# Kernel optimization log

Measured on AMD Instinct MI355X. Metric: run time of the kernel, lower is better.

## Reference

```python
import jax, jax.numpy as jnp
import numpy as np

V_TH = 1.0
V_RESET = 0.0
BN_EPS = 1e-5

# Heaviside spike with ATan surrogate gradient (spikingjelly surrogate.ATan, alpha=2)
@jax.custom_vjp
def spike(x):
    return (x >= 0).astype(x.dtype)

def _spike_fwd(x):
    return spike(x), x

def _spike_bwd(x, g):
    alpha = 2.0
    sg = (alpha / 2.0) / (1.0 + (jnp.pi / 2.0 * alpha * x) ** 2)
    return (g * sg,)

spike.defvjp(_spike_fwd, _spike_bwd)


def lif_block(x, w, W, b, gamma, beta):
    """LTLIF (learnable tau, decay_input=False, hard reset) -> Linear -> BatchNorm1d.
    x: [T, B, C]"""
    inv_tau = jax.nn.sigmoid(w)  # 1/tau, learnable via w

    def step(v, xt):
        # decay_input=False charge: v = v - (v - v_reset)/tau + x_t
        v = v - (v - V_RESET) * inv_tau + xt
        s = spike(v - V_TH)
        v = (1.0 - s) * v + s * V_RESET  # hard reset
        return v, s

    v0 = jnp.full(x.shape[1:], V_RESET, dtype=x.dtype)
    _, spikes = jax.lax.scan(step, v0, x)  # spikes: [T, B, C]

    y = jnp.einsum('tbc,dc->tbd', spikes, W) + b  # Linear per step
    # BatchNorm1d in multi-step mode: stats over flattened (T*B) per channel
    mean = jnp.mean(y, axis=(0, 1))
    var = jnp.var(y, axis=(0, 1))
    y = (y - mean) * jax.lax.rsqrt(var + BN_EPS) * gamma + beta
    return y


def setup_inputs() -> dict:
    key = jax.random.key(0)
    ks = jax.random.split(key, 3)
    T, B, C = 128, 256, 512
    scale = 1.0 / np.sqrt(C)
    return {
        'x': jax.random.normal(ks[0], (T, B, C), jnp.float32),
        'w0': jnp.zeros((), jnp.float32),  # sigmoid(0)=0.5 => tau=2
        'W0': jax.random.normal(ks[1], (C, C), jnp.float32) * scale,
        'b0': jnp.zeros((C,), jnp.float32),
        'gamma0': jnp.ones((C,), jnp.float32),
        'beta0': jnp.zeros((C,), jnp.float32),
        'w1': jnp.zeros((), jnp.float32),
        'W1': jax.random.normal(ks[2], (C, C), jnp.float32) * scale,
        'b1': jnp.zeros((C,), jnp.float32),
        'gamma1': jnp.ones((C,), jnp.float32),
        'beta1': jnp.zeros((C,), jnp.float32),
    }


def reference(x, w0, W0, b0, gamma0, beta0, w1, W1, b1, gamma1, beta1):
    h = lif_block(x, w0, W0, b0, gamma0, beta0)   # process block (Dropout p=0 -> identity)
    h = lif_block(h, w1, W1, b1, gamma1, beta1)   # out block
    return h + x  # skip_connect=True
```

## Files before the change

### kernel.cpp

```cpp
#include <hip/hip_runtime.h>


typedef int i32x4 __attribute__((ext_vector_type(4)));

#define T_STEPS 128
#define BATCH   256
#define CH      512
#define BC      (BATCH * CH)
#define MROWS   (T_STEPS * BATCH)

__device__ __forceinline__ void llds16(const void* g, void* l) {
  __builtin_amdgcn_global_load_lds(
      (const __attribute__((address_space(1))) void*)g,
      (__attribute__((address_space(3))) void*)l, 16, 0, 0);
}

__device__ __forceinline__ unsigned lds_off(const void* p) {
  return (unsigned)(size_t)(__attribute__((address_space(3))) const void*)p;
}

__device__ __forceinline__ i32x4 ds128(unsigned off) {
  i32x4 r;
  asm volatile("ds_read_b128 %0, %1" : "=v"(r) : "v"(off));
  return r;
}

__global__ __launch_bounds__(256) void k_convw(const float* __restrict__ W0,
                                               const float* __restrict__ W1,
                                               signed char* __restrict__ WL0,
                                               signed char* __restrict__ WL1) {
  int b = blockIdx.x;
  const float* W = (b < 1024) ? W0 : W1;
  signed char* WL = (b < 1024) ? WL0 : WL1;
  int i = (b & 1023) * 256 + threadIdx.x;
  double z = (double)W[i] * 4294967296.0;
  z = fmin(fmax(z, -2147483647.0), 2147483647.0);
  int q = (int)llrint(z);
  int r = q;
  signed char l0 = (signed char)r; r = (r - l0) >> 8;
  signed char l1 = (signed char)r; r = (r - l1) >> 8;
  signed char l2 = (signed char)r; r = (r - l2) >> 8;
  signed char l3 = (signed char)r;
  WL[i]          = l0;
  WL[i + 262144] = l1;
  WL[i + 524288] = l2;
  WL[i + 786432] = l3;
}

__global__ __launch_bounds__(64) void k_lif1(const float* __restrict__ X,
                                             const float* __restrict__ wp,
                                             signed char* __restrict__ S) {
  int i = blockIdx.x * 64 + threadIdx.x;
  float om = 1.0f - 1.0f / (1.0f + expf(-wp[0]));
  float v = 0.0f;
  #pragma unroll 8
  for (int t = 0; t < T_STEPS; ++t) {
    float xt = X[(size_t)t * BC + i];
    v = v * om + xt;
    bool sp = (v >= 1.0f);
    S[(size_t)t * BC + i] = sp;
    v = sp ? 0.0f : v;
  }
}

__global__ __launch_bounds__(64) void k_lif2(const float* __restrict__ Y,
                                             const double* __restrict__ sA,
                                             const double* __restrict__ sB,
                                             const float* __restrict__ wp,
                                             signed char* __restrict__ S) {
  int i = blockIdx.x * 64 + threadIdx.x;
  int c = i & (CH - 1);
  double a = sA[c], b = sB[c];
  float om = 1.0f - 1.0f / (1.0f + expf(-wp[0]));
  float v = 0.0f;
  #pragma unroll 8
  for (int t = 0; t < T_STEPS; ++t) {
    float h = (float)((double)Y[(size_t)t * BC + i] * a + b);
    v = v * om + h;
    bool sp = (v >= 1.0f);
    S[(size_t)t * BC + i] = sp;
    v = sp ? 0.0f : v;
  }
}

__global__ __launch_bounds__(256, 3) void k_gemm(const signed char* __restrict__ S,
                                                 const signed char* __restrict__ WL,
                                                 float* __restrict__ Y,
                                                 double* __restrict__ sumP,
                                                 double* __restrict__ sqP) {
  __shared__ __align__(16) signed char Bb[2][4][64 * 64];

  const int tid  = threadIdx.x;
  const int wid  = tid >> 6;
  const int lane = tid & 63;
  const int bid   = blockIdx.x;
  const int xcd   = bid & 7;
  const int local = bid >> 3;
  const int bn    = local & 7;
  const int bm    = xcd * 64 + (local >> 3);
  const int m0 = bm * 64, n0 = bn * 64;
  const int wm = wid >> 1, wn = wid & 1;
  const int lr = lane & 15, lg = lane >> 4;

  i32x4 acc[2][2][4] = {};

  auto STAGE = [&](int buf, int kt) {
    int row = tid >> 2, gl = tid & 3;
    int gg = gl ^ ((row >> 1) & 3);
    #pragma unroll
    for (int j = 0; j < 4; ++j)
      llds16(WL + (size_t)j * 262144 + (size_t)(n0 + row) * 512 + kt + gg * 16,
             (char*)Bb[buf][j] + wid * 1024);
  };

  const unsigned bbase = lds_off(&Bb[0][0][0]);
  unsigned voff[2];
  #pragma unroll
  for (int n = 0; n < 2; ++n) {
    int r = wn * 32 + n * 16 + lr;
    int g = lg ^ ((r >> 1) & 3);
    voff[n] = bbase + (unsigned)(r * 64 + g * 16);
  }

  const signed char* aP = S + (size_t)(m0 + wm * 32 + lr) * 512 + lg * 16;

  STAGE(0, 0);

  #pragma unroll
  for (int i = 0; i < 8; ++i) {
    const int cur = i & 1;

    i32x4 a[2];
    #pragma unroll
    for (int m = 0; m < 2; ++m)
      a[m] = *(const i32x4*)(aP + m * 8192 + i * 64);

    if (i < 7) STAGE(cur ^ 1, (i + 1) * 64);

    if (i < 7) asm volatile("s_waitcnt vmcnt(6)" ::: "memory");
    else       asm volatile("s_waitcnt vmcnt(2)" ::: "memory");
    asm volatile("s_barrier" ::: "memory");

    i32x4 b[2][2];
    #pragma unroll
    for (int n = 0; n < 2; ++n)
      #pragma unroll
      for (int j = 0; j < 2; ++j)
        b[n][j] = ds128(voff[n] + (unsigned)(cur * 16384 + j * 4096));

    if (i < 7) asm volatile("s_waitcnt vmcnt(4)" ::: "memory");
    else       asm volatile("s_waitcnt vmcnt(0)" ::: "memory");
    asm volatile("s_waitcnt lgkmcnt(0)" ::: "memory");
    __builtin_amdgcn_sched_barrier(0);

    __builtin_amdgcn_s_setprio(1);
    #pragma unroll
    for (int j = 0; j < 2; ++j)
      #pragma unroll
      for (int m = 0; m < 2; ++m)
        #pragma unroll
        for (int n = 0; n < 2; ++n)
          acc[m][n][j] = __builtin_amdgcn_mfma_i32_16x16x64_i8(
              a[m], b[n][j], acc[m][n][j], 0, 0, 0);

    i32x4 b2[2][2];
    #pragma unroll
    for (int n = 0; n < 2; ++n)
      #pragma unroll
      for (int j = 0; j < 2; ++j)
        b2[n][j] = ds128(voff[n] + (unsigned)(cur * 16384 + (j + 2) * 4096));
    asm volatile("s_waitcnt lgkmcnt(0)" ::: "memory");
    __builtin_amdgcn_sched_barrier(0);

    #pragma unroll
    for (int j = 0; j < 2; ++j)
      #pragma unroll
      for (int m = 0; m < 2; ++m)
        #pragma unroll
        for (int n = 0; n < 2; ++n)
          acc[m][n][j + 2] = __builtin_amdgcn_mfma_i32_16x16x64_i8(
              a[m], b2[n][j], acc[m][n][j + 2], 0, 0, 0);
    __builtin_amdgcn_s_setprio(0);

    asm volatile("s_barrier" ::: "memory");
  }

  const int r0 = m0 + wm * 32 + lg * 4;
  const int cl = wn * 32 + lr;
  double s0 = 0, q0 = 0, s1 = 0, q1 = 0;
  #pragma unroll
  for (int m = 0; m < 2; ++m)
    #pragma unroll
    for (int n = 0; n < 2; ++n)
      #pragma unroll
      for (int q = 0; q < 4; ++q) {
        double yv = (((double)acc[m][n][3][q] * 256.0 + (double)acc[m][n][2][q]) * 256.0
                     + (double)acc[m][n][1][q]) * 256.0 + (double)acc[m][n][0][q];
        float yf = (float)(yv * 0x1p-32);
        Y[(size_t)(r0 + m * 16 + q) * 512 + n0 + cl + n * 16] = yf;
        double yd = (double)yf;
        if (n == 0) { s0 += yd; q0 += yd * yd; }
        else        { s1 += yd; q1 += yd * yd; }
      }
  s0 += __shfl_xor(s0, 16); s0 += __shfl_xor(s0, 32);
  q0 += __shfl_xor(q0, 16); q0 += __shfl_xor(q0, 32);
  s1 += __shfl_xor(s1, 16); s1 += __shfl_xor(s1, 32);
  q1 += __shfl_xor(q1, 16); q1 += __shfl_xor(q1, 32);

  double* shS = (double*)Bb[0][0];
  double* shQ = shS + 128;
  __syncthreads();
  if (lane < 16) {
    shS[wm * 64 + cl]      = s0;  shQ[wm * 64 + cl]      = q0;
    shS[wm * 64 + cl + 16] = s1;  shQ[wm * 64 + cl + 16] = q1;
  }
  __syncthreads();
  if (tid < 64) {
    sumP[(size_t)(n0 + tid) * 512 + bm] = shS[tid] + shS[64 + tid];
    sqP [(size_t)(n0 + tid) * 512 + bm] = shQ[tid] + shQ[64 + tid];
  }
}

__global__ __launch_bounds__(256) void k_stats2(const double* __restrict__ sumP,
                                                const double* __restrict__ sqP,
                                                const float* __restrict__ gamma,
                                                const float* __restrict__ beta,
                                                double* __restrict__ sA,
                                                double* __restrict__ sB) {
  __shared__ double shS[256], shQ[256];
  int c = blockIdx.x;
  int t = threadIdx.x;
  shS[t] = sumP[(size_t)c * 512 + t] + sumP[(size_t)c * 512 + t + 256];
  shQ[t] = sqP [(size_t)c * 512 + t] + sqP [(size_t)c * 512 + t + 256];
  __syncthreads();
  for (int w = 128; w >= 1; w >>= 1) {
    if (t < w) { shS[t] += shS[t + w]; shQ[t] += shQ[t + w]; }
    __syncthreads();
  }
  if (t == 0) {
    const double invN = 1.0 / 32768.0;
    double mean = shS[0] * invN;
    double var  = shQ[0] * invN - mean * mean;
    double rstd = rsqrt(var + 1e-5);
    double a = (double)gamma[c] * rstd;
    sA[c] = a;
    sB[c] = (double)beta[c] - mean * a;
  }
}

__global__ __launch_bounds__(256) void k_final(float* __restrict__ Y,
                                               const float* __restrict__ X,
                                               const double* __restrict__ sA,
                                               const double* __restrict__ sB) {
  size_t i = (size_t)blockIdx.x * 256 + threadIdx.x;
  int c0 = (int)((i * 4) & (CH - 1));
  float4 y = ((const float4*)Y)[i];
  float4 x = ((const float4*)X)[i];
  float4 o;
  o.x = (float)((double)y.x * sA[c0 + 0] + sB[c0 + 0] + (double)x.x);
  o.y = (float)((double)y.y * sA[c0 + 1] + sB[c0 + 1] + (double)x.y);
  o.z = (float)((double)y.z * sA[c0 + 2] + sB[c0 + 2] + (double)x.z);
  o.w = (float)((double)y.w * sA[c0 + 3] + sB[c0 + 3] + (double)x.w);
  ((float4*)Y)[i] = o;
}

extern "C" void kernel_launch(void* const* d_in, const int* in_sizes, int n_in,
                              void* d_out, int out_size, void* d_ws, size_t ws_size,
                              hipStream_t stream) {
  (void)in_sizes; (void)n_in; (void)out_size; (void)ws_size;

  const float* x   = (const float*)d_in[0];
  const float* w0  = (const float*)d_in[1];
  const float* W0  = (const float*)d_in[2];
  const float* g0  = (const float*)d_in[4];
  const float* be0 = (const float*)d_in[5];
  const float* w1  = (const float*)d_in[6];
  const float* W1  = (const float*)d_in[7];
  const float* g1  = (const float*)d_in[9];
  const float* be1 = (const float*)d_in[10];
  float* Y = (float*)d_out;

  char* ws = (char*)d_ws;
  signed char* WL0  = (signed char*)(ws + 0x0000000);
  signed char* WL1  = (signed char*)(ws + 0x0100000);
  signed char* spk  = (signed char*)(ws + 0x0200000);
  double*      sumP = (double*)(ws + 0x1200000);
  double*      sqP  = (double*)(ws + 0x1400000);
  double*      sA   = (double*)(ws + 0x1600000);
  double*      sB   = (double*)(ws + 0x1602000);

  k_convw<<<2048, 256, 0, stream>>>(W0, W1, WL0, WL1);

  k_lif1 <<<BC / 64, 64, 0, stream>>>(x, w0, spk);
  k_gemm <<<(MROWS / 64) * (CH / 64), 256, 0, stream>>>(spk, WL0, Y, sumP, sqP);
  k_stats2<<<512, 256, 0, stream>>>(sumP, sqP, g0, be0, sA, sB);

  k_lif2 <<<BC / 64, 64, 0, stream>>>(Y, sA, sB, w1, spk);
  k_gemm <<<(MROWS / 64) * (CH / 64), 256, 0, stream>>>(spk, WL1, Y, sumP, sqP);
  k_stats2<<<512, 256, 0, stream>>>(sumP, sqP, g1, be1, sA, sB);

  k_final<<<(MROWS * CH) / (4 * 256), 256, 0, stream>>>(Y, x, sA, sB);
}
```

Baseline: 192.9 us.

## Split int8 GEMM waves over weight byte-planes instead of M rows

The int8 GEMM block's four waves now split the work by weight byte-plane pairs instead of by M rows. Each wave covers all 64 rows with 4 A fragments and 2 byte-planes, where before it covered 32 rows with 4 byte-planes. The two wave groups combine their partial plane sums through LDS before the Y store and the BN statistics. Each wave now reads only half of the B tile from LDS but loads twice as many A rows from global memory, and launch bounds are raised to 4 blocks per CU. The epilogue gains an extra LDS round trip and barrier, and the higher occupancy target constrains register usage.

```diff
diff --git a/kernel.cpp b/kernel.cpp
--- a/kernel.cpp
+++ b/kernel.cpp
@@ -83,7 +83,7 @@
   }
 }
 
-__global__ __launch_bounds__(256, 3) void k_gemm(const signed char* __restrict__ S,
+__global__ __launch_bounds__(256, 4) void k_gemm(const signed char* __restrict__ S,
                                                  const signed char* __restrict__ WL,
                                                  float* __restrict__ Y,
                                                  double* __restrict__ sumP,
@@ -102,7 +102,7 @@
   const int wm = wid >> 1, wn = wid & 1;
   const int lr = lane & 15, lg = lane >> 4;
 
-  i32x4 acc[2][2][4] = {};
+  i32x4 acc[4][2][2] = {};
 
   auto STAGE = [&](int buf, int kt) {
     int row = tid >> 2, gl = tid & 3;
@@ -113,7 +113,7 @@
              (char*)Bb[buf][j] + wid * 1024);
   };
 
-  const unsigned bbase = lds_off(&Bb[0][0][0]);
+  const unsigned bbase = lds_off(&Bb[0][0][0]) + (unsigned)(wm * 2) * 4096;
   unsigned voff[2];
   #pragma unroll
   for (int n = 0; n < 2; ++n) {
@@ -122,7 +122,7 @@
     voff[n] = bbase + (unsigned)(r * 64 + g * 16);
   }
 
-  const signed char* aP = S + (size_t)(m0 + wm * 32 + lr) * 512 + lg * 16;
+  const signed char* aP = S + (size_t)(m0 + lr) * 512 + lg * 16;
 
   STAGE(0, 0);
 
@@ -130,23 +130,23 @@
   for (int i = 0; i < 8; ++i) {
     const int cur = i & 1;
 
-    i32x4 a[2];
-    #pragma unroll
-    for (int m = 0; m < 2; ++m)
+    i32x4 a[4];
+    #pragma unroll
+    for (int m = 0; m < 4; ++m)
       a[m] = *(const i32x4*)(aP + m * 8192 + i * 64);
 
     if (i < 7) STAGE(cur ^ 1, (i + 1) * 64);
 
-    if (i < 7) asm volatile("s_waitcnt vmcnt(6)" ::: "memory");
-    else       asm volatile("s_waitcnt vmcnt(2)" ::: "memory");
+    if (i < 7) asm volatile("s_waitcnt vmcnt(8)" ::: "memory");
+    else       asm volatile("s_waitcnt vmcnt(4)" ::: "memory");
     asm volatile("s_barrier" ::: "memory");
 
     i32x4 b[2][2];
     #pragma unroll
     for (int n = 0; n < 2; ++n)
       #pragma unroll
-      for (int j = 0; j < 2; ++j)
-        b[n][j] = ds128(voff[n] + (unsigned)(cur * 16384 + j * 4096));
+      for (int jj = 0; jj < 2; ++jj)
+        b[n][jj] = ds128(voff[n] + (unsigned)(cur * 16384 + jj * 4096));
 
     if (i < 7) asm volatile("s_waitcnt vmcnt(4)" ::: "memory");
     else       asm volatile("s_waitcnt vmcnt(0)" ::: "memory");
@@ -155,69 +155,70 @@
 
     __builtin_amdgcn_s_setprio(1);
     #pragma unroll
-    for (int j = 0; j < 2; ++j)
+    for (int jj = 0; jj < 2; ++jj)
       #pragma unroll
-      for (int m = 0; m < 2; ++m)
+      for (int m = 0; m < 4; ++m)
         #pragma unroll
         for (int n = 0; n < 2; ++n)
-          acc[m][n][j] = __builtin_amdgcn_mfma_i32_16x16x64_i8(
-              a[m], b[n][j], acc[m][n][j], 0, 0, 0);
-
-    i32x4 b2[2][2];
-    #pragma unroll
-    for (int n = 0; n < 2; ++n)
+          acc[m][n][jj] = __builtin_amdgcn_mfma_i32_16x16x64_i8(
+              a[m], b[n][jj], acc[m][n][jj], 0, 0, 0);
+    __builtin_amdgcn_s_setprio(0);
+
+    asm volatile("s_barrier" ::: "memory");
+  }
+
+  const int rowL = lg * 4;
+  const int colL = wn * 32 + lr;
+  double* comb = (double*)Bb;
+
+  __syncthreads();
+  if (wm == 1) {
+    #pragma unroll
+    for (int m = 0; m < 4; ++m)
       #pragma unroll
-      for (int j = 0; j < 2; ++j)
-        b2[n][j] = ds128(voff[n] + (unsigned)(cur * 16384 + (j + 2) * 4096));
-    asm volatile("s_waitcnt lgkmcnt(0)" ::: "memory");
-    __builtin_amdgcn_sched_barrier(0);
-
-    #pragma unroll
-    for (int j = 0; j < 2; ++j)
+      for (int n = 0; n < 2; ++n)
+        #pragma unroll
+        for (int q = 0; q < 4; ++q)
+          comb[(m * 16 + rowL + q) * 64 + colL + n * 16] =
+              65536.0 * ((double)acc[m][n][0][q] + 256.0 * (double)acc[m][n][1][q]);
+  }
+  __syncthreads();
+  double s[2] = {0, 0}, qs[2] = {0, 0};
+  if (wm == 0) {
+    #pragma unroll
+    for (int m = 0; m < 4; ++m)
       #pragma unroll
-      for (int m = 0; m < 2; ++m)
+      for (int n = 0; n < 2; ++n)
         #pragma unroll
-        for (int n = 0; n < 2; ++n)
-          acc[m][n][j + 2] = __builtin_amdgcn_mfma_i32_16x16x64_i8(
-              a[m], b2[n][j], acc[m][n][j + 2], 0, 0, 0);
-    __builtin_amdgcn_s_setprio(0);
-
-    asm volatile("s_barrier" ::: "memory");
-  }
-
-  const int r0 = m0 + wm * 32 + lg * 4;
-  const int cl = wn * 32 + lr;
-  double s0 = 0, q0 = 0, s1 = 0, q1 = 0;
-  #pragma unroll
-  for (int m = 0; m < 2; ++m)
-    #pragma unroll
-    for (int n = 0; n < 2; ++n)
-      #pragma unroll
-      for (int q = 0; q < 4; ++q) {
-        double yv = (((double)acc[m][n][3][q] * 256.0 + (double)acc[m][n][2][q]) * 256.0
-                     + (double)acc[m][n][1][q]) * 256.0 + (double)acc[m][n][0][q];
-        float yf = (float)(yv * 0x1p-32);
-        Y[(size_t)(r0 + m * 16 + q) * 512 + n0 + cl + n * 16] = yf;
-        double yd = (double)yf;
-        if (n == 0) { s0 += yd; q0 += yd * yd; }
-        else        { s1 += yd; q1 += yd * yd; }
-      }
-  s0 += __shfl_xor(s0, 16); s0 += __shfl_xor(s0, 32);
-  q0 += __shfl_xor(q0, 16); q0 += __shfl_xor(q0, 32);
-  s1 += __shfl_xor(s1, 16); s1 += __shfl_xor(s1, 32);
-  q1 += __shfl_xor(q1, 16); q1 += __shfl_xor(q1, 32);
-
-  double* shS = (double*)Bb[0][0];
-  double* shQ = shS + 128;
-  __syncthreads();
-  if (lane < 16) {
-    shS[wm * 64 + cl]      = s0;  shQ[wm * 64 + cl]      = q0;
-    shS[wm * 64 + cl + 16] = s1;  shQ[wm * 64 + cl + 16] = q1;
+        for (int q = 0; q < 4; ++q) {
+          int row = m * 16 + rowL + q;
+          double yv = (double)acc[m][n][0][q] + 256.0 * (double)acc[m][n][1][q]
+                      + comb[row * 64 + colL + n * 16];
+          float yf = (float)(yv * 0x1p-32);
+          Y[(size_t)(m0 + row) * 512 + n0 + colL + n * 16] = yf;
+          double yd = (double)yf;
+          s[n] += yd; qs[n] += yd * yd;
+        }
+    #pragma unroll
+    for (int n = 0; n < 2; ++n) {
+      s[n]  += __shfl_xor(s[n], 16);  s[n]  += __shfl_xor(s[n], 32);
+      qs[n] += __shfl_xor(qs[n], 16); qs[n] += __shfl_xor(qs[n], 32);
+    }
+  }
+  __syncthreads();
+  double* shS = (double*)Bb;
+  double* shQ = shS + 64;
+  if (wm == 0 && lane < 16) {
+    #pragma unroll
+    for (int n = 0; n < 2; ++n) {
+      shS[wn * 32 + n * 16 + lane] = s[n];
+      shQ[wn * 32 + n * 16 + lane] = qs[n];
+    }
   }
   __syncthreads();
   if (tid < 64) {
-    sumP[(size_t)(n0 + tid) * 512 + bm] = shS[tid] + shS[64 + tid];
-    sqP [(size_t)(n0 + tid) * 512 + bm] = shQ[tid] + shQ[64 + tid];
+    sumP[(size_t)(n0 + tid) * 512 + bm] = shS[tid];
+    sqP [(size_t)(n0 + tid) * 512 + bm] = shQ[tid];
   }
 }
 
```

Result: slower. 282.1 us (+46.2%).
